# Kernel optimization log

Hardware: AMD Instinct MI355X
Metric: run time of the kernel (lower is better)

## Reference

```python
import jax, jax.numpy as jnp
import numpy as np
import math

IN_CH = 1024
OUT_CH = 512
T_DIM = 512
CLIP = 8
HEADS = 8
BS = 8192


def setup_inputs() -> dict:
    key = jax.random.key(0)
    ks = jax.random.split(key, 12)
    s = 0.02
    return {
        "x": jax.random.normal(ks[0], (BS * CLIP, IN_CH), dtype=jnp.float32),
        "t": jax.random.normal(ks[1], (BS, 1, T_DIM), dtype=jnp.float32),
        "W_down": jax.random.normal(ks[2], (OUT_CH, IN_CH), dtype=jnp.float32) * s,
        "b_down": jax.random.normal(ks[3], (OUT_CH,), dtype=jnp.float32) * s,
        "W_t": jax.random.normal(ks[4], (OUT_CH, T_DIM), dtype=jnp.float32) * s,
        "b_t": jax.random.normal(ks[5], (OUT_CH,), dtype=jnp.float32) * s,
        "W_qkv": jax.random.normal(ks[6], (3 * OUT_CH, OUT_CH), dtype=jnp.float32) * s,
        "b_qkv": jax.random.normal(ks[7], (3 * OUT_CH,), dtype=jnp.float32) * s,
        "W_out": jax.random.normal(ks[8], (OUT_CH, OUT_CH), dtype=jnp.float32) * s,
        "b_out": jax.random.normal(ks[9], (OUT_CH,), dtype=jnp.float32) * s,
    }


def reference(x, t, W_down, b_down, W_t, b_t, W_qkv, b_qkv, W_out, b_out):
    # down projection (in_channel != out_channels branch)
    x = x @ W_down.T + b_down                       # [bs*clip, out_ch]
    x = x.reshape(-1, CLIP, OUT_CH)                 # [bs, clip, out_ch]
    # time embedding (broadcast over clip dim)
    x = x + (t @ W_t.T + b_t)                       # [bs, clip, out_ch]
    qkv = x @ W_qkv.T + b_qkv                       # [bs, clip, 3*out_ch]
    bs, length, width = qkv.shape
    ch = width // (3 * HEADS)                       # 64
    q, k, v = jnp.split(qkv, 3, axis=2)             # each [bs, clip, out_ch]
    scale = 1.0 / math.sqrt(math.sqrt(ch))
    # NOTE: faithful to torch .view semantics (head-interleaved reshape)
    qh = (q * scale).reshape(bs * HEADS, length, ch)
    kh = (k * scale).reshape(bs * HEADS, length, ch)
    vh = v.reshape(bs * HEADS, length, ch)
    w = jnp.einsum('bqc,bkc->bqk', qh, kh)          # [bs*heads, clip, clip]
    w = jax.nn.softmax(w.astype(jnp.float32), axis=-1).astype(qkv.dtype)
    attn = jnp.einsum('bqk,bkc->bqc', w, vh).reshape(bs, length, -1)
    return attn @ W_out.T + b_out                   # [bs, clip, out_ch]
```

## Files before the change

kernel.cpp:

```cpp
#include <hip/hip_runtime.h>
#include <hip/hip_bf16.h>
#include <cstdint>
#include <cstddef>

typedef __bf16 bf16_t;
typedef __bf16 bf16x8 __attribute__((ext_vector_type(8)));
typedef float  f32x4  __attribute__((ext_vector_type(4)));

#define N_ROWS 65536
#define IN_CH  1024
#define OUT_CH 512
#define T_DIM  512
#define BS_    8192

__device__ __forceinline__ void async_copy16(const bf16_t* g, bf16_t* l) {
    __builtin_amdgcn_global_load_lds(
        (const __attribute__((address_space(1))) void*)(uintptr_t)(g),
        (__attribute__((address_space(3))) void*)(uintptr_t)(l),
        16, 0, 0);
}

__global__ __launch_bounds__(256)
void cvt_f32_bf16(const float* __restrict__ in, bf16_t* __restrict__ out, long n8) {
    long idx = (long)blockIdx.x * 256 + threadIdx.x;
    if (idx >= n8) return;
    const float4* p = (const float4*)(in + idx * 8);
    float4 u = p[0], v = p[1];
    bf16x8 o;
    o[0] = (__bf16)u.x; o[1] = (__bf16)u.y; o[2] = (__bf16)u.z; o[3] = (__bf16)u.w;
    o[4] = (__bf16)v.x; o[5] = (__bf16)v.y; o[6] = (__bf16)v.z; o[7] = (__bf16)v.w;
    *(bf16x8*)(out + idx * 8) = o;
}

template<int BIAS_MODE, typename CT>
__global__ __launch_bounds__(256, 2)
void gemm_bt(const bf16_t* __restrict__ A, const bf16_t* __restrict__ B,
             CT* __restrict__ C,
             const float* __restrict__ bias,
             const float* __restrict__ bias2,
             int M, int N, int K)
{
    __shared__ bf16_t sA[128 * 32];
    __shared__ bf16_t sB[128 * 32];

    const int tid  = threadIdx.x;
    const int wave = tid >> 6;
    const int lane = tid & 63;

    const int row0 = blockIdx.y * 128;
    const int col0 = blockIdx.x * 128;

    const int wr = (wave >> 1) * 64;
    const int wc = (wave & 1) * 64;

    f32x4 acc[4][4];
    #pragma unroll
    for (int i = 0; i < 4; ++i)
        #pragma unroll
        for (int j = 0; j < 4; ++j)
            acc[i][j] = (f32x4){0.f, 0.f, 0.f, 0.f};

    const int seg0  = wave * 2;
    const int srow  = lane >> 2;
    const int schnk = (lane & 3) * 8;

    const bf16_t* Abase = A + (size_t)row0 * K + (size_t)srow * K + schnk;
    const bf16_t* Bbase = B + (size_t)col0 * K + (size_t)srow * K + schnk;

    const int fr = lane & 15;
    const int fk = (lane >> 4) * 8;

    for (int k0 = 0; k0 < K; k0 += 32) {
        #pragma unroll
        for (int j2 = 0; j2 < 2; ++j2) {
            const int seg = seg0 + j2;
            async_copy16(Abase + (size_t)(seg * 16) * K + k0, sA + seg * 512);
            async_copy16(Bbase + (size_t)(seg * 16) * K + k0, sB + seg * 512);
        }
        __syncthreads();

        bf16x8 af[4], bfr[4];
        #pragma unroll
        for (int i = 0; i < 4; ++i)
            af[i] = *(const bf16x8*)(sA + (wr + i * 16 + fr) * 32 + fk);
        #pragma unroll
        for (int j = 0; j < 4; ++j)
            bfr[j] = *(const bf16x8*)(sB + (wc + j * 16 + fr) * 32 + fk);

        #pragma unroll
        for (int i = 0; i < 4; ++i)
            #pragma unroll
            for (int j = 0; j < 4; ++j)
                acc[i][j] = __builtin_amdgcn_mfma_f32_16x16x32_bf16(af[i], bfr[j], acc[i][j], 0, 0, 0);
        __syncthreads();
    }

    #pragma unroll
    for (int j = 0; j < 4; ++j) {
        const int gc = col0 + wc + j * 16 + (lane & 15);
        float cb = 0.f;
        if constexpr (BIAS_MODE == 0) cb = bias[gc];
        if constexpr (BIAS_MODE == 2) cb = bias[gc] + bias2[gc];
        #pragma unroll
        for (int i = 0; i < 4; ++i) {
            const int gr0 = row0 + wr + i * 16 + ((lane >> 4) << 2);
            #pragma unroll
            for (int r = 0; r < 4; ++r) {
                const int gr = gr0 + r;
                float v = acc[i][j][r];
                if constexpr (BIAS_MODE == 1)
                    v += bias2[(size_t)(gr >> 3) * N + gc];
                else
                    v += cb;
                C[(size_t)gr * N + gc] = (CT)v;
            }
        }
    }
}

__global__ __launch_bounds__(256, 4)
void attn_kernel(const bf16_t* __restrict__ qkv, bf16_t* __restrict__ out)
{
    __shared__ bf16_t skv[4][1024];
    const int tid  = threadIdx.x;
    const int wave = tid >> 6;
    const int lane = tid & 63;
    const size_t row = (size_t)blockIdx.x * 4 + wave;

    const bf16_t* base = qkv + row * 1536;
    bf16x8 q8 = *(const bf16x8*)(base + lane * 8);
    bf16x8 k8 = *(const bf16x8*)(base + 512 + lane * 8);
    bf16x8 v8 = *(const bf16x8*)(base + 1024 + lane * 8);
    *(bf16x8*)&skv[wave][lane * 8]       = k8;
    *(bf16x8*)&skv[wave][512 + lane * 8] = v8;

    float q[8];
    #pragma unroll
    for (int e = 0; e < 8; ++e) q[e] = (float)q8[e];
    __syncthreads();

    const int s8 = (lane & 7) * 8;
    float S[8];
    #pragma unroll
    for (int j = 0; j < 8; ++j) {
        bf16x8 kj = *(const bf16x8*)&skv[wave][j * 64 + s8];
        float p = 0.f;
        #pragma unroll
        for (int e = 0; e < 8; ++e) p += q[e] * (float)kj[e];
        p += __shfl_xor(p, 1);
        p += __shfl_xor(p, 2);
        p += __shfl_xor(p, 4);
        S[j] = p * 0.125f;
    }
    float m = S[0];
    #pragma unroll
    for (int j = 1; j < 8; ++j) m = fmaxf(m, S[j]);
    float sum = 0.f;
    #pragma unroll
    for (int j = 0; j < 8; ++j) { S[j] = __expf(S[j] - m); sum += S[j]; }
    const float inv = 1.f / sum;

    float o[8] = {0.f, 0.f, 0.f, 0.f, 0.f, 0.f, 0.f, 0.f};
    #pragma unroll
    for (int j = 0; j < 8; ++j) {
        const float pj = S[j] * inv;
        bf16x8 vj = *(const bf16x8*)&skv[wave][512 + j * 64 + s8];
        #pragma unroll
        for (int e = 0; e < 8; ++e) o[e] += pj * (float)vj[e];
    }
    bf16x8 o8;
    #pragma unroll
    for (int e = 0; e < 8; ++e) o8[e] = (__bf16)o[e];
    *(bf16x8*)(out + row * 512 + lane * 8) = o8;
}

extern "C" void kernel_launch(void* const* d_in, const int* in_sizes, int n_in,
                              void* d_out, int out_size, void* d_ws, size_t ws_size,
                              hipStream_t stream)
{
    const float* x      = (const float*)d_in[0];
    const float* t      = (const float*)d_in[1];
    const float* W_down = (const float*)d_in[2];
    const float* b_down = (const float*)d_in[3];
    const float* W_t    = (const float*)d_in[4];
    const float* b_t    = (const float*)d_in[5];
    const float* W_qkv  = (const float*)d_in[6];
    const float* b_qkv  = (const float*)d_in[7];
    const float* W_out  = (const float*)d_in[8];
    const float* b_out  = (const float*)d_in[9];
    float* out = (float*)d_out;

    char* p = (char*)d_ws;
    bf16_t* xb    = (bf16_t*)(p);
    bf16_t* qkvm  = (bf16_t*)(p);
    bf16_t* x1    = (bf16_t*)(p + 201326592);
    bf16_t* am    = (bf16_t*)(p + 268435456);
    bf16_t* tb16  = (bf16_t*)(p + 335544320);
    float*  tbias = (float*) (p + 343932928);
    bf16_t* wd    = (bf16_t*)(p + 360710144);
    bf16_t* wt    = (bf16_t*)(p + 361758720);
    bf16_t* wq    = (bf16_t*)(p + 362283008);
    bf16_t* wo    = (bf16_t*)(p + 363855872);

    cvt_f32_bf16<<<32768, 256, 0, stream>>>(x, xb, (long)N_ROWS * IN_CH / 8);
    cvt_f32_bf16<<<2048, 256, 0, stream>>>(t, tb16, (long)BS_ * T_DIM / 8);
    cvt_f32_bf16<<<256, 256, 0, stream>>>(W_down, wd, (long)OUT_CH * IN_CH / 8);
    cvt_f32_bf16<<<128, 256, 0, stream>>>(W_t, wt, (long)OUT_CH * T_DIM / 8);
    cvt_f32_bf16<<<384, 256, 0, stream>>>(W_qkv, wq, (long)3 * OUT_CH * OUT_CH / 8);
    cvt_f32_bf16<<<128, 256, 0, stream>>>(W_out, wo, (long)OUT_CH * OUT_CH / 8);

    gemm_bt<2, float><<<dim3(4, 64), 256, 0, stream>>>(
        tb16, wt, tbias, b_t, b_down, BS_, OUT_CH, T_DIM);

    gemm_bt<1, bf16_t><<<dim3(4, 512), 256, 0, stream>>>(
        xb, wd, x1, nullptr, tbias, N_ROWS, OUT_CH, IN_CH);

    gemm_bt<0, bf16_t><<<dim3(12, 512), 256, 0, stream>>>(
        x1, wq, qkvm, b_qkv, nullptr, N_ROWS, 3 * OUT_CH, OUT_CH);

    attn_kernel<<<16384, 256, 0, stream>>>(qkvm, am);

    gemm_bt<0, float><<<dim3(4, 512), 256, 0, stream>>>(
        am, wo, out, b_out, nullptr, N_ROWS, OUT_CH, OUT_CH);
}
```

Measured before the change: 804.7 us.

## Fold down-projection weights into QKV weights and fuse time bias per batch

Precomputes a fused weight Wf = W_qkv·W_down (1536x1024, stored bf16) using a transposed bf16 copy of W_down. The time embedding is pushed through W_qkv once per batch element to form a per-batch float bias. The down-projection GEMM and its x1 intermediate are replaced by one larger GEMM from x straight to qkv, which adds the per-batch bias in its epilogue. This removes a kernel and the x1 round trip through memory, but the main GEMM now does more multiply-adds (K=1024 with N=1536) and the fused weights are rounded to bf16. GEMM launch bounds also go from 2 to 3 waves per SIMD hint.

Result: slower. 873.4 us (+8.5%).

```diff
diff --git a/kernel.cpp b/kernel.cpp
--- a/kernel.cpp
+++ b/kernel.cpp
@@ -32,8 +32,45 @@
     *(bf16x8*)(out + idx * 8) = o;
 }
 
+__global__ __launch_bounds__(256)
+void cvt_multi(const float* __restrict__ s0, bf16_t* __restrict__ d0, long n0,
+               const float* __restrict__ s1, bf16_t* __restrict__ d1, long n1,
+               const float* __restrict__ s2, bf16_t* __restrict__ d2, long n2,
+               const float* __restrict__ s3, bf16_t* __restrict__ d3, long n3)
+{
+    long idx = (long)blockIdx.x * 256 + threadIdx.x;
+    const float* s; bf16_t* d;
+    if (idx < n0)                { s = s0; d = d0; }
+    else if ((idx -= n0) < n1)   { s = s1; d = d1; }
+    else if ((idx -= n1) < n2)   { s = s2; d = d2; }
+    else if ((idx -= n2) < n3)   { s = s3; d = d3; }
+    else return;
+    const float4* p = (const float4*)(s + idx * 8);
+    float4 u = p[0], v = p[1];
+    bf16x8 o;
+    o[0] = (__bf16)u.x; o[1] = (__bf16)u.y; o[2] = (__bf16)u.z; o[3] = (__bf16)u.w;
+    o[4] = (__bf16)v.x; o[5] = (__bf16)v.y; o[6] = (__bf16)v.z; o[7] = (__bf16)v.w;
+    *(bf16x8*)(d + idx * 8) = o;
+}
+
+__global__ __launch_bounds__(256)
+void transpose_cvt(const float* __restrict__ in, bf16_t* __restrict__ out) {
+    __shared__ float tile[64][65];
+    const int bx = blockIdx.x;
+    const int by = blockIdx.y;
+    const int tx = threadIdx.x & 63;
+    const int ty = threadIdx.x >> 6;
+    #pragma unroll
+    for (int r = 0; r < 64; r += 4)
+        tile[r + ty][tx] = in[(size_t)(by * 64 + r + ty) * 1024 + bx * 64 + tx];
+    __syncthreads();
+    #pragma unroll
+    for (int r = 0; r < 64; r += 4)
+        out[(size_t)(bx * 64 + r + ty) * 512 + by * 64 + tx] = (bf16_t)tile[tx][r + ty];
+}
+
 template<int BIAS_MODE, typename CT>
-__global__ __launch_bounds__(256, 2)
+__global__ __launch_bounds__(256, 3)
 void gemm_bt(const bf16_t* __restrict__ A, const bf16_t* __restrict__ B,
              CT* __restrict__ C,
              const float* __restrict__ bias,
@@ -191,32 +228,37 @@
     float* out = (float*)d_out;
 
     char* p = (char*)d_ws;
-    bf16_t* xb    = (bf16_t*)(p);
-    bf16_t* qkvm  = (bf16_t*)(p);
-    bf16_t* x1    = (bf16_t*)(p + 201326592);
-    bf16_t* am    = (bf16_t*)(p + 268435456);
-    bf16_t* tb16  = (bf16_t*)(p + 335544320);
-    float*  tbias = (float*) (p + 343932928);
-    bf16_t* wd    = (bf16_t*)(p + 360710144);
-    bf16_t* wt    = (bf16_t*)(p + 361758720);
-    bf16_t* wq    = (bf16_t*)(p + 362283008);
-    bf16_t* wo    = (bf16_t*)(p + 363855872);
+    bf16_t* xb     = (bf16_t*)(p);
+    bf16_t* qkvm   = (bf16_t*)(p + 134217728);
+    bf16_t* am     = (bf16_t*)(p + 335544320);
+    float*  tbias2 = (float*) (p + 402653184);
+    bf16_t* tin    = (bf16_t*)(p + 452984832);
+    bf16_t* tb     = (bf16_t*)(p + 461373440);
+    bf16_t* wdT    = (bf16_t*)(p + 469762048);
+    bf16_t* wt     = (bf16_t*)(p + 470810624);
+    bf16_t* wq     = (bf16_t*)(p + 471334912);
+    bf16_t* wo     = (bf16_t*)(p + 472907776);
+    bf16_t* wf     = (bf16_t*)(p + 473432064);
 
     cvt_f32_bf16<<<32768, 256, 0, stream>>>(x, xb, (long)N_ROWS * IN_CH / 8);
-    cvt_f32_bf16<<<2048, 256, 0, stream>>>(t, tb16, (long)BS_ * T_DIM / 8);
-    cvt_f32_bf16<<<256, 256, 0, stream>>>(W_down, wd, (long)OUT_CH * IN_CH / 8);
-    cvt_f32_bf16<<<128, 256, 0, stream>>>(W_t, wt, (long)OUT_CH * T_DIM / 8);
-    cvt_f32_bf16<<<384, 256, 0, stream>>>(W_qkv, wq, (long)3 * OUT_CH * OUT_CH / 8);
-    cvt_f32_bf16<<<128, 256, 0, stream>>>(W_out, wo, (long)OUT_CH * OUT_CH / 8);
-
-    gemm_bt<2, float><<<dim3(4, 64), 256, 0, stream>>>(
-        tb16, wt, tbias, b_t, b_down, BS_, OUT_CH, T_DIM);
-
-    gemm_bt<1, bf16_t><<<dim3(4, 512), 256, 0, stream>>>(
-        xb, wd, x1, nullptr, tbias, N_ROWS, OUT_CH, IN_CH);
-
-    gemm_bt<0, bf16_t><<<dim3(12, 512), 256, 0, stream>>>(
-        x1, wq, qkvm, b_qkv, nullptr, N_ROWS, 3 * OUT_CH, OUT_CH);
+    cvt_multi<<<2688, 256, 0, stream>>>(
+        t,     tin, (long)BS_ * T_DIM / 8,
+        W_qkv, wq,  (long)3 * OUT_CH * OUT_CH / 8,
+        W_t,   wt,  (long)OUT_CH * T_DIM / 8,
+        W_out, wo,  (long)OUT_CH * OUT_CH / 8);
+    transpose_cvt<<<dim3(16, 8), 256, 0, stream>>>(W_down, wdT);
+
+    gemm_bt<3, bf16_t><<<dim3(8, 12), 256, 0, stream>>>(
+        wq, wdT, wf, nullptr, nullptr, 3 * OUT_CH, IN_CH, OUT_CH);
+
+    gemm_bt<2, bf16_t><<<dim3(4, 64), 256, 0, stream>>>(
+        tin, wt, tb, b_t, b_down, BS_, OUT_CH, T_DIM);
+
+    gemm_bt<0, float><<<dim3(12, 64), 256, 0, stream>>>(
+        tb, wq, tbias2, b_qkv, nullptr, BS_, 3 * OUT_CH, OUT_CH);
+
+    gemm_bt<1, bf16_t><<<dim3(12, 512), 256, 0, stream>>>(
+        xb, wf, qkvm, nullptr, tbias2, N_ROWS, 3 * OUT_CH, IN_CH);
 
     attn_kernel<<<16384, 256, 0, stream>>>(qkvm, am);
 
```
